# Kernel optimization log

Measured on AMD Instinct MI355X. Metric: run time of the kernel, lower is better.

The kernel has to match this reference:

```python
import jax, jax.numpy as jnp
import numpy as np
import math

DIM_IN = 512
DIM_OUT = 512
KERNEL = 3
STYLE_DIM = 2 * 128
LIN_SCALE = 1.0 / math.sqrt(STYLE_DIM)      # EqualLinear scale (lr_mul=1)
CONV_SCALE = 1.0 / math.sqrt(DIM_IN * KERNEL ** 2)  # fan_in = dim_in * k**2 (as in source)
PAD = KERNEL // 2


def setup_inputs() -> dict:
    key = jax.random.key(0)
    ks = jax.random.split(key, 5)
    B, T = 16, 2048
    x = jax.random.normal(ks[0], (B, DIM_IN, T), dtype=jnp.float32)
    c_src = jax.random.normal(ks[1], (B, 128), dtype=jnp.float32)
    c_trg = jax.random.normal(ks[2], (B, 128), dtype=jnp.float32)
    style_w = jax.random.normal(ks[3], (DIM_IN, STYLE_DIM), dtype=jnp.float32)
    style_b = jnp.ones((DIM_IN,), dtype=jnp.float32)  # bias_init=1
    weight = jax.random.normal(ks[4], (1, DIM_OUT, DIM_IN, KERNEL), dtype=jnp.float32)
    return {"x": x, "c_src": c_src, "c_trg": c_trg,
            "style_w": style_w, "style_b": style_b, "weight": weight}


def reference(x, c_src, c_trg, style_w, style_b, weight):
    B = x.shape[0]
    # EqualLinear: style code s [B, dim_in]
    c = jnp.concatenate([c_src, c_trg], axis=-1)              # [B, 256]
    s = c @ (style_w * LIN_SCALE).T + style_b                 # [B, dim_in]
    # Modulate: w [B, dim_out, dim_in, k]
    w = CONV_SCALE * weight * s[:, None, :, None]
    # Demodulate over (dim_in, k)
    demod = jax.lax.rsqrt(jnp.sum(w * w, axis=(2, 3)) + 1e-8)  # [B, dim_out]
    w = w * demod[:, :, None, None]
    # Per-sample conv1d, padding 'same' (pad = k//2), vmapped over batch
    def conv1(xi, wi):
        # xi: [dim_in, T], wi: [dim_out, dim_in, k]
        out = jax.lax.conv_general_dilated(
            xi[None], wi, window_strides=(1,), padding=[(PAD, PAD)],
            dimension_numbers=("NCH", "OIH", "NCH"))
        return out[0]                                          # [dim_out, T]
    return jax.vmap(conv1)(x, w)                               # [B, dim_out, T]
```

## Files before the change

### kernel.cpp

```cpp
#include <hip/hip_runtime.h>
#include <cstdint>
#include <cstddef>


#define LIN_SCALE  0.0625f
#define CONV_SCALE 0.014731391f

#define B_   16
#define CIN  512
#define COUT 512
#define T_   2048
#define TP   2050

typedef __bf16 bf16x8 __attribute__((ext_vector_type(8)));
typedef float  f32x4  __attribute__((ext_vector_type(4)));
typedef unsigned short u16x8 __attribute__((ext_vector_type(8)));
typedef unsigned short u16x2 __attribute__((ext_vector_type(2)));

#define AS1 __attribute__((address_space(1)))
#define AS3 __attribute__((address_space(3)))

__device__ inline unsigned short f2bf(float f) {
  __bf16 h = (__bf16)f;
  return __builtin_bit_cast(unsigned short, h);
}

__global__ __launch_bounds__(256) void style_kernel(const float* __restrict__ c_src,
                                                    const float* __restrict__ c_trg,
                                                    const float* __restrict__ sw,
                                                    const float* __restrict__ sb,
                                                    float* __restrict__ s) {
  __shared__ float c[256];
  const int b = blockIdx.y;
  const int tid = threadIdx.x;
  c[tid] = (tid < 128) ? c_src[b * 128 + tid] : c_trg[b * 128 + tid - 128];
  __syncthreads();
  const int w = tid >> 6, lane = tid & 63;
  #pragma unroll
  for (int rr = 0; rr < 16; ++rr) {
    const int i = blockIdx.x * 64 + w * 16 + rr;
    const float* row = sw + (size_t)i * 256;
    float acc = row[lane] * c[lane] + row[lane + 64] * c[lane + 64]
              + row[lane + 128] * c[lane + 128] + row[lane + 192] * c[lane + 192];
    #pragma unroll
    for (int off = 32; off; off >>= 1) acc += __shfl_down(acc, off, 64);
    if (lane == 0) s[b * 512 + i] = acc * LIN_SCALE + sb[i];
  }
}

__global__ __launch_bounds__(256) void demod_kernel(const float* __restrict__ weight,
                                                    const float* __restrict__ s,
                                                    float* __restrict__ demod,
                                                    unsigned short* __restrict__ Wb) {
  const int o = blockIdx.x;
  const int tid = threadIdx.x;
  __shared__ float wsh[1536];
  __shared__ float svs[16 * 512];
  __shared__ float partial[16][4];

  #pragma unroll
  for (int j = tid; j < 384; j += 256)
    ((float4*)wsh)[j] = ((const float4*)(weight + (size_t)o * 1536))[j];
  #pragma unroll
  for (int j = tid; j < 2048; j += 256)
    ((float4*)svs)[j] = ((const float4*)s)[j];
  __syncthreads();

  float wr[6];
  #pragma unroll
  for (int q = 0; q < 6; ++q) wr[q] = wsh[tid * 6 + q] * CONV_SCALE;

  #pragma unroll
  for (int k = 0; k < 3; ++k) {
    u16x2 v;
    v.x = f2bf(wr[k]);
    v.y = f2bf(wr[3 + k]);
    *(u16x2*)&Wb[((size_t)(k * 512 + o)) * 512 + 2 * tid] = v;
  }

  const int lane = tid & 63, w = tid >> 6;
  float ssb[16];
  #pragma unroll
  for (int b = 0; b < 16; ++b) {
    const float s0 = svs[b * 512 + 2 * tid];
    const float s1 = svs[b * 512 + 2 * tid + 1];
    float ss = 0.f;
    #pragma unroll
    for (int q = 0; q < 3; ++q) { float v = wr[q] * s0; ss += v * v; }
    #pragma unroll
    for (int q = 3; q < 6; ++q) { float v = wr[q] * s1; ss += v * v; }
    ssb[b] = ss;
  }
  #pragma unroll
  for (int b = 0; b < 16; ++b) {
    float ss = ssb[b];
    #pragma unroll
    for (int off = 32; off; off >>= 1) ss += __shfl_down(ss, off, 64);
    if (lane == 0) partial[b][w] = ss;
  }
  __syncthreads();
  if (tid < 16)
    demod[(size_t)tid * 512 + o] =
        rsqrtf(partial[tid][0] + partial[tid][1] + partial[tid][2] + partial[tid][3] + 1e-8f);
}

__global__ __launch_bounds__(256) void transpose_kernel(const float* __restrict__ x,
                                                        const float* __restrict__ s,
                                                        unsigned short* __restrict__ xT) {
  __shared__ float tile[64][65];
  __shared__ float ss[64];
  const int b = blockIdx.z, i0 = blockIdx.y * 64, t0 = blockIdx.x * 64;
  const int tid = threadIdx.x;

  if (tid < 64) ss[tid] = s[(size_t)b * 512 + i0 + tid];

  const int lr = tid >> 4;
  const int lc = (tid & 15) * 4;
  const float* xb = x + ((size_t)b * CIN + i0) * T_ + t0;
  #pragma unroll
  for (int p = 0; p < 4; ++p) {
    const int r = p * 16 + lr;
    const float4 v = *(const float4*)(xb + (size_t)r * T_ + lc);
    tile[r][lc + 0] = v.x; tile[r][lc + 1] = v.y;
    tile[r][lc + 2] = v.z; tile[r][lc + 3] = v.w;
  }
  if (blockIdx.x == 0 && tid < 8)
    *(u16x8*)&xT[(size_t)b * TP * CIN + i0 + tid * 8] = (u16x8){0,0,0,0,0,0,0,0};
  if (blockIdx.x == gridDim.x - 1 && tid < 8)
    *(u16x8*)&xT[((size_t)b * TP + TP - 1) * CIN + i0 + tid * 8] = (u16x8){0,0,0,0,0,0,0,0};
  __syncthreads();

  const int st = tid >> 3;
  const int si = (tid & 7) * 8;
  float sv[8];
  #pragma unroll
  for (int q = 0; q < 8; ++q) sv[q] = ss[si + q];
  unsigned short* xTb = xT + ((size_t)b * TP + 1 + t0) * CIN + i0;
  #pragma unroll
  for (int p = 0; p < 2; ++p) {
    const int t = p * 32 + st;
    u16x8 v;
    #pragma unroll
    for (int q = 0; q < 8; ++q) v[q] = f2bf(tile[si + q][t] * sv[q]);
    *(u16x8*)&xTb[(size_t)t * CIN + si] = v;
  }
}

#define VMCNT0  asm volatile("s_waitcnt vmcnt(0)" ::: "memory")

#define STAGEB(buf, i0g) do {                                                 \
    _Pragma("unroll")                                                         \
    for (int q = 0; q < 4; ++q) {                                             \
      const int ci  = q * 256 + tid;                                          \
      const int row = ci >> 2;                                                \
      const int gc  = ((ci & 3) ^ ((row >> 1) & 3)) * 8;                      \
      __builtin_amdgcn_global_load_lds(                                       \
          (const AS1 void*)(gX + (size_t)row * CIN + (i0g) + gc),             \
          (AS3 void*)(&lB[buf][ci * 8]), 16, 0, 0);                           \
    }                                                                         \
    if (tid < 8) {                                                            \
      const int ci  = 1024 + tid;                                             \
      const int row = ci >> 2;                                                \
      const int gc  = ((ci & 3) ^ ((row >> 1) & 3)) * 8;                      \
      __builtin_amdgcn_global_load_lds(                                       \
          (const AS1 void*)(gX + (size_t)row * CIN + (i0g) + gc),             \
          (AS3 void*)(&lB[buf][ci * 8]), 16, 0, 0);                           \
    }                                                                         \
  } while (0)

__global__ __launch_bounds__(256, 2) void gemm_kernel(const unsigned short* __restrict__ Wb,
                                                      const unsigned short* __restrict__ xT,
                                                      const float* __restrict__ demod,
                                                      float* __restrict__ out) {
  __shared__ unsigned short lB[2][1032 * 8];

  const int id  = blockIdx.x;
  const int xcd = id & 7;
  const int j   = id >> 3;
  const int b   = xcd + 8 * (j >> 5);
  const int r   = j & 31;
  const int o0  = (r >> 3) * 128;
  const int t0  = (r & 7) * 256;

  const int tid  = threadIdx.x;
  const int lane = tid & 63;
  const int wt   = ((tid >> 6) & 1) * 128;
  const int wo   = (tid >> 7) * 64;
  const int rl   = lane & 15;
  const int kc   = lane >> 4;

  const unsigned short* gWl = Wb + ((size_t)(o0 + wo + rl)) * 512 + kc * 8;
  const unsigned short* gX  = xT + ((size_t)b * TP + t0) * CIN;

  f32x4 acc[8][4];
  #pragma unroll
  for (int i = 0; i < 8; ++i)
    #pragma unroll
    for (int jj = 0; jj < 4; ++jj) acc[i][jj] = (f32x4){0.f, 0.f, 0.f, 0.f};

  STAGEB(0, 0);
  VMCNT0;
  __builtin_amdgcn_s_barrier();

  for (int kk = 0; kk < 16; ++kk) {
    const int i0  = kk * 32;
    const int cur = kk & 1;
    if (kk < 15) STAGEB(cur ^ 1, i0 + 32);

    bf16x8 wf[3][4];
    #pragma unroll
    for (int tap = 0; tap < 3; ++tap)
      #pragma unroll
      for (int ni = 0; ni < 4; ++ni)
        wf[tap][ni] = *(const bf16x8*)(gWl + (size_t)tap * 262144 + ni * 8192 + i0);

    #pragma unroll
    for (int tap = 0; tap < 3; ++tap) {
      bf16x8 xf[8];
      #pragma unroll
      for (int mi = 0; mi < 8; ++mi) {
        const int rb = wt + mi * 16 + rl + tap;
        xf[mi] = *(const bf16x8*)&lB[cur][(rb * 4 + (kc ^ ((rb >> 1) & 3))) * 8];
      }
      #pragma unroll
      for (int mi = 0; mi < 8; ++mi)
        #pragma unroll
        for (int ni = 0; ni < 4; ++ni)
          acc[mi][ni] = __builtin_amdgcn_mfma_f32_16x16x32_bf16(xf[mi], wf[tap][ni], acc[mi][ni], 0, 0, 0);
    }

    VMCNT0;
    __builtin_amdgcn_s_barrier();
  }

  const int ccol = lane & 15;
  const int trow = (lane >> 4) * 4;
  float dmv[4];
  #pragma unroll
  for (int ni = 0; ni < 4; ++ni)
    dmv[ni] = demod[(size_t)b * 512 + o0 + wo + ni * 16 + ccol];
  float* ob = out + ((size_t)b * COUT + o0 + wo + ccol) * T_ + t0 + wt + trow;
  #pragma unroll
  for (int mi = 0; mi < 8; ++mi)
    #pragma unroll
    for (int ni = 0; ni < 4; ++ni) {
      f32x4 v = acc[mi][ni];
      v.x *= dmv[ni]; v.y *= dmv[ni]; v.z *= dmv[ni]; v.w *= dmv[ni];
      *(f32x4*)&ob[(size_t)ni * 16 * T_ + mi * 16] = v;
    }
}

extern "C" void kernel_launch(void* const* d_in, const int* in_sizes, int n_in,
                              void* d_out, int out_size, void* d_ws, size_t ws_size,
                              hipStream_t stream) {
  const float* x       = (const float*)d_in[0];
  const float* c_src   = (const float*)d_in[1];
  const float* c_trg   = (const float*)d_in[2];
  const float* style_w = (const float*)d_in[3];
  const float* style_b = (const float*)d_in[4];
  const float* weight  = (const float*)d_in[5];
  float* out = (float*)d_out;

  char* ws = (char*)d_ws;
  float* s_buf          = (float*)ws;
  float* demod_buf      = (float*)(ws + 32768);
  unsigned short* Wb    = (unsigned short*)(ws + 65536);
  unsigned short* xTbuf = (unsigned short*)(ws + 65536 + 1572864);

  style_kernel<<<dim3(8, 16), 256, 0, stream>>>(c_src, c_trg, style_w, style_b, s_buf);
  demod_kernel<<<dim3(COUT), 256, 0, stream>>>(weight, s_buf, demod_buf, Wb);
  transpose_kernel<<<dim3(T_ / 64, CIN / 64, B_), 256, 0, stream>>>(x, s_buf, xTbuf);
  gemm_kernel<<<dim3(512), 256, 0, stream>>>(Wb, xTbuf, demod_buf, out);
}
```

Measured before the change: 196.6 us.

## Stage weights through LDS and enlarge GEMM tile to 128x512 with 8 waves

The weight fragments were previously loaded straight from global memory each k-step. They are now staged into double-buffered LDS alongside the x tile. The block tile grows to 128 output channels by 512 timesteps with 512 threads, which halves the grid to 256 blocks and raises per-block reuse. MFMA sections are wrapped in s_setprio, and the output store changes to scalar writes along rows. The risks are lower occupancy and fewer blocks than CUs, the larger LDS footprint, and less vectorised stores.

Result: faster. 186.9 us (-5.0%).

```diff
diff --git a/kernel.cpp b/kernel.cpp
--- a/kernel.cpp
+++ b/kernel.cpp
@@ -151,7 +151,7 @@
 #define STAGEB(buf, i0g) do {                                                 \
     _Pragma("unroll")                                                         \
     for (int q = 0; q < 4; ++q) {                                             \
-      const int ci  = q * 256 + tid;                                          \
+      const int ci  = q * 512 + tid;                                          \
       const int row = ci >> 2;                                                \
       const int gc  = ((ci & 3) ^ ((row >> 1) & 3)) * 8;                      \
       __builtin_amdgcn_global_load_lds(                                       \
@@ -159,95 +159,110 @@
           (AS3 void*)(&lB[buf][ci * 8]), 16, 0, 0);                           \
     }                                                                         \
     if (tid < 8) {                                                            \
-      const int ci  = 1024 + tid;                                             \
-      const int row = ci >> 2;                                                \
+      const int ci  = 2048 + tid;                                             \
+      const int row = ci >> 2;                                  \
       const int gc  = ((ci & 3) ^ ((row >> 1) & 3)) * 8;                      \
       __builtin_amdgcn_global_load_lds(                                       \
           (const AS1 void*)(gX + (size_t)row * CIN + (i0g) + gc),             \
           (AS3 void*)(&lB[buf][ci * 8]), 16, 0, 0);                           \
-    }                                                                         \
-  } while (0)
-
-__global__ __launch_bounds__(256, 2) void gemm_kernel(const unsigned short* __restrict__ Wb,
+    } } while (0)
+
+#define STAGEA(buf, i0g) do {                                                 \
+    _Pragma("unroll")                                                         \
+    for (int q = 0; q < 3; ++q) {                                             \
+      const int ci  = q * 512 + tid;                                          \
+      const int row = ci >> 2;                              \
+      const int tap = row >> 7;                                               \
+      const int ar  = row & 127;                                              \
+      const int gc  = ((ci & 3) ^ ((ar >> 1) & 3)) * 8;                       \
+      __builtin_amdgcn_global_load_lds(                                       \
+          (const AS1 void*)(gW + (size_t)tap * 262144 + (size_t)ar * 512 + (i0g) + gc), \
+          (AS3 void*)(&lA[buf][ci * 8]), 16, 0, 0);                           \
+    } } while (0)
+
+__global__ __launch_bounds__(512, 2) void gemm_kernel(const unsigned short* __restrict__ Wb,
                                                       const unsigned short* __restrict__ xT,
                                                       const float* __restrict__ demod,
                                                       float* __restrict__ out) {
-  __shared__ unsigned short lB[2][1032 * 8];
+  __shared__ unsigned short lA[2][1536 * 8];
+  __shared__ unsigned short lB[2][2056 * 8];
 
   const int id  = blockIdx.x;
   const int xcd = id & 7;
   const int j   = id >> 3;
-  const int b   = xcd + 8 * (j >> 5);
-  const int r   = j & 31;
-  const int o0  = (r >> 3) * 128;
-  const int t0  = (r & 7) * 256;
+  const int b   = xcd + 8 * (j >> 4);
+  const int r   = j & 15;
+  const int o0  = (r >> 2) * 128;
+  const int t0  = (r & 3) * 512;
 
   const int tid  = threadIdx.x;
   const int lane = tid & 63;
-  const int wt   = ((tid >> 6) & 1) * 128;
-  const int wo   = (tid >> 7) * 64;
+  const int wid  = tid >> 6;
+  const int wm   = (wid & 1) * 64;
+  const int wn   = (wid >> 1) * 128;
   const int rl   = lane & 15;
   const int kc   = lane >> 4;
 
-  const unsigned short* gWl = Wb + ((size_t)(o0 + wo + rl)) * 512 + kc * 8;
-  const unsigned short* gX  = xT + ((size_t)b * TP + t0) * CIN;
-
-  f32x4 acc[8][4];
-  #pragma unroll
-  for (int i = 0; i < 8; ++i)
-    #pragma unroll
-    for (int jj = 0; jj < 4; ++jj) acc[i][jj] = (f32x4){0.f, 0.f, 0.f, 0.f};
+  const unsigned short* gW = Wb + (size_t)o0 * 512;
+  const unsigned short* gX = xT + ((size_t)b * TP + t0) * CIN;
+
+  f32x4 acc[4][8];
+  #pragma unroll
+  for (int i = 0; i < 4; ++i)
+    #pragma unroll
+    for (int jj = 0; jj < 8; ++jj) acc[i][jj] = (f32x4){0.f, 0.f, 0.f, 0.f};
 
   STAGEB(0, 0);
+  STAGEA(0, 0);
   VMCNT0;
   __builtin_amdgcn_s_barrier();
 
   for (int kk = 0; kk < 16; ++kk) {
-    const int i0  = kk * 32;
     const int cur = kk & 1;
-    if (kk < 15) STAGEB(cur ^ 1, i0 + 32);
-
-    bf16x8 wf[3][4];
-    #pragma unroll
-    for (int tap = 0; tap < 3; ++tap)
-      #pragma unroll
-      for (int ni = 0; ni < 4; ++ni)
-        wf[tap][ni] = *(const bf16x8*)(gWl + (size_t)tap * 262144 + ni * 8192 + i0);
-
+    if (kk < 15) {
+      STAGEB(cur ^ 1, (kk + 1) * 32);
+      STAGEA(cur ^ 1, (kk + 1) * 32);
+    }
     #pragma unroll
     for (int tap = 0; tap < 3; ++tap) {
-      bf16x8 xf[8];
-      #pragma unroll
-      for (int mi = 0; mi < 8; ++mi) {
-        const int rb = wt + mi * 16 + rl + tap;
-        xf[mi] = *(const bf16x8*)&lB[cur][(rb * 4 + (kc ^ ((rb >> 1) & 3))) * 8];
+      bf16x8 af[4], bfr[8];
+      #pragma unroll
+      for (int mi = 0; mi < 4; ++mi) {
+        const int ra = wm + mi * 16 + rl;
+        af[mi] = *(const bf16x8*)&lA[cur][((tap * 128 + ra) * 4 + (kc ^ ((ra >> 1) & 3))) * 8];
       }
       #pragma unroll
-      for (int mi = 0; mi < 8; ++mi)
+      for (int ni = 0; ni < 8; ++ni) {
+        const int rb = wn + ni * 16 + rl + tap;
+        bfr[ni] = *(const bf16x8*)&lB[cur][(rb * 4 + (kc ^ ((rb >> 1) & 3))) * 8];
+      }
+      __builtin_amdgcn_s_setprio(1);
+      #pragma unroll
+      for (int mi = 0; mi < 4; ++mi)
         #pragma unroll
-        for (int ni = 0; ni < 4; ++ni)
-          acc[mi][ni] = __builtin_amdgcn_mfma_f32_16x16x32_bf16(xf[mi], wf[tap][ni], acc[mi][ni], 0, 0, 0);
+        for (int ni = 0; ni < 8; ++ni)
+          acc[mi][ni] = __builtin_amdgcn_mfma_f32_16x16x32_bf16(af[mi], bfr[ni], acc[mi][ni], 0, 0, 0);
+      __builtin_amdgcn_s_setprio(0);
     }
-
     VMCNT0;
     __builtin_amdgcn_s_barrier();
   }
 
+  float* ob = out + ((size_t)b * COUT + o0 + wm) * T_ + t0 + wn;
+  const float* dm = demod + (size_t)b * 512 + o0 + wm;
+  const int rrow = (lane >> 4) * 4;
   const int ccol = lane & 15;
-  const int trow = (lane >> 4) * 4;
-  float dmv[4];
-  #pragma unroll
-  for (int ni = 0; ni < 4; ++ni)
-    dmv[ni] = demod[(size_t)b * 512 + o0 + wo + ni * 16 + ccol];
-  float* ob = out + ((size_t)b * COUT + o0 + wo + ccol) * T_ + t0 + wt + trow;
-  #pragma unroll
-  for (int mi = 0; mi < 8; ++mi)
-    #pragma unroll
-    for (int ni = 0; ni < 4; ++ni) {
-      f32x4 v = acc[mi][ni];
-      v.x *= dmv[ni]; v.y *= dmv[ni]; v.z *= dmv[ni]; v.w *= dmv[ni];
-      *(f32x4*)&ob[(size_t)ni * 16 * T_ + mi * 16] = v;
-    }
+  #pragma unroll
+  for (int mi = 0; mi < 4; ++mi) {
+    float dr[4];
+    #pragma unroll
+    for (int rr = 0; rr < 4; ++rr) dr[rr] = dm[mi * 16 + rrow + rr];
+    #pragma unroll
+    for (int ni = 0; ni < 8; ++ni)
+      #pragma unroll
+      for (int rr = 0; rr < 4; ++rr)
+        ob[(size_t)(mi * 16 + rrow + rr) * T_ + ni * 16 + ccol] = acc[mi][ni][rr] * dr[rr];
+  }
 }
 
 extern "C" void kernel_launch(void* const* d_in, const int* in_sizes, int n_in,
@@ -270,5 +285,5 @@
   style_kernel<<<dim3(8, 16), 256, 0, stream>>>(c_src, c_trg, style_w, style_b, s_buf);
   demod_kernel<<<dim3(COUT), 256, 0, stream>>>(weight, s_buf, demod_buf, Wb);
   transpose_kernel<<<dim3(T_ / 64, CIN / 64, B_), 256, 0, stream>>>(x, s_buf, xTbuf);
-  gemm_kernel<<<dim3(512), 256, 0, stream>>>(Wb, xTbuf, demod_buf, out);
-}
+  gemm_kernel<<<dim3(256), 512, 0, stream>>>(Wb, xTbuf, demod_buf, out);
+}
```
